# Performance work log

Hardware: AMD Instinct MI355X
Metric: run time of the kernel (lower is better)

The kernel has to match this reference:

```python
import jax, jax.numpy as jnp
import numpy as np

N = 100000      # nodes
E = 1600000     # directed edges
F_IN = 9        # atom features (fixed by GCNConv(9, hidden))
H = 128         # hidden_channels
G = 64          # graphs in batch


def setup_inputs() -> dict:
    key = jax.random.key(0)
    ks = jax.random.split(key, 12)
    x = jax.random.normal(ks[0], (N, F_IN), dtype=jnp.float32)
    edge_index = jax.random.randint(ks[1], (2, E), 0, N, dtype=jnp.int64)
    batch = jnp.sort(jax.random.randint(ks[2], (N,), 0, G, dtype=jnp.int64))
    def lin_init(k, fan_in, fan_out):
        s = 1.0 / np.sqrt(fan_in)
        kw, kb = jax.random.split(k)
        W = jax.random.uniform(kw, (fan_in, fan_out), jnp.float32, -s, s)
        b = jax.random.uniform(kb, (fan_out,), jnp.float32, -s, s)
        return W, b
    W1, b1 = lin_init(ks[3], F_IN, H)
    W2, b2 = lin_init(ks[4], H, H)
    W3, b3 = lin_init(ks[5], H, H)
    lin_w, lin_b = lin_init(ks[6], H, 1)
    return {"x": x, "edge_index": edge_index, "batch": batch,
            "W1": W1, "b1": b1, "W2": W2, "b2": b2, "W3": W3, "b3": b3,
            "lin_w": lin_w, "lin_b": lin_b}


def reference(x, edge_index, batch, W1, b1, W2, b2, W3, b3, lin_w, lin_b):
    n = x.shape[0]
    # PyG GCNConv default: add self-loops, symmetric normalization D^-1/2 (A+I) D^-1/2
    loops = jnp.arange(n, dtype=edge_index.dtype)
    src = jnp.concatenate([edge_index[0], loops])   # [E+N]
    dst = jnp.concatenate([edge_index[1], loops])   # [E+N]
    deg = jax.ops.segment_sum(jnp.ones_like(dst, dtype=x.dtype), dst, num_segments=n)
    dinv = jnp.where(deg > 0, jax.lax.rsqrt(jnp.maximum(deg, 1e-12)), 0.0)
    norm = (dinv[src] * dinv[dst])[:, None]         # [E+N, 1]

    def gcn_conv(h, W, b):
        hw = h @ W                                   # [N, H]
        msg = hw[src] * norm                         # gather + scale  [E+N, H]
        return jax.ops.segment_sum(msg, dst, num_segments=n) + b  # scatter-add

    h = jax.nn.relu(gcn_conv(x, W1, b1))
    h = jax.nn.relu(gcn_conv(h, W2, b2))
    h = gcn_conv(h, W3, b3)

    # global_mean_pool over graph ids
    counts = jax.ops.segment_sum(jnp.ones((n,), x.dtype), batch, num_segments=G)
    pooled = jax.ops.segment_sum(h, batch, num_segments=G) / jnp.maximum(counts, 1.0)[:, None]
    return pooled @ lin_w + lin_b                    # [G, 1]
```

## Files before the change

kernel.cpp:

```cpp
#include <hip/hip_runtime.h>
#include <math.h>


#define CHUNK 2048

using short8 = __attribute__((ext_vector_type(8))) short;
using floatx4 = __attribute__((ext_vector_type(4))) float;

__device__ __forceinline__ int rankof(int i, int nq, int nr) {
  int c = i & 7;
  return c * nq + min(c, nr) + (i >> 3);
}
__device__ __forceinline__ unsigned int f2bf(float f) {
  unsigned int u = __float_as_uint(f);
  return ((u + 0x7fff + ((u >> 16) & 1)) >> 16);
}
__device__ __forceinline__ float bflo(unsigned int u) { return __uint_as_float(u << 16); }
__device__ __forceinline__ float bfhi(unsigned int u) { return __uint_as_float(u & 0xffff0000u); }


__global__ void deg_kernel(const int* __restrict__ dst, int* cnt_rank,
                           int E, int nq, int nr) {
  int e = blockIdx.x * blockDim.x + threadIdx.x;
  if (e < E) atomicAdd(&cnt_rank[rankof(dst[e], nq, nr)], 1);
}

__global__ void dinv_bsum_pad_kernel(const int* __restrict__ cnt_rank,
                                     float* __restrict__ dinv, int* bsum,
                                     const float* __restrict__ x,
                                     unsigned short* __restrict__ xp, int N, int nq, int nr) {
  __shared__ int s[256];
  int t = threadIdx.x;
  int gid = blockIdx.x * 256 + t;
  s[t] = (gid < N) ? cnt_rank[gid] : 0;
  if (gid < N) {
    int c = cnt_rank[rankof(gid, nq, nr)];
    float di = 1.0f / sqrtf((float)c + 1.0f);
    dinv[gid] = di;
    const float* xr = x + (size_t)gid * 9;
    unsigned int w0 = f2bf(xr[0] * di) | (f2bf(xr[1] * di) << 16);
    unsigned int w1 = f2bf(xr[2] * di) | (f2bf(xr[3] * di) << 16);
    unsigned int w2 = f2bf(xr[4] * di) | (f2bf(xr[5] * di) << 16);
    unsigned int w3 = f2bf(xr[6] * di) | (f2bf(xr[7] * di) << 16);
    unsigned int w4 = f2bf(xr[8] * di);
    uint4* xo = (uint4*)(xp + (size_t)gid * 16);
    xo[0] = make_uint4(w0, w1, w2, w3);
    xo[1] = make_uint4(w4, 0u, 0u, 0u);
  }
  __syncthreads();
  for (int off = 128; off > 0; off >>= 1) {
    if (t < off) s[t] += s[t + off];
    __syncthreads();
  }
  if (t == 0) bsum[blockIdx.x] = s[0];
}

__global__ void rowptr_vc0_kernel(const int* __restrict__ indeg, const int* __restrict__ bsum,
                                  int2* __restrict__ rows, int* cursor, int N, int E,
                                  int nq, int nr,
                                  const float* __restrict__ W3, const float* __restrict__ b3,
                                  const float* __restrict__ lin_w, const float* __restrict__ lin_b,
                                  const float* __restrict__ W2, unsigned short* __restrict__ W2p,
                                  unsigned short* __restrict__ g,
                                  float* v, float* c0) {
  __shared__ int ps[256];
  __shared__ int s[256];
  int t = threadIdx.x;
  int pref = 0;
  for (int q = t; q < blockIdx.x; q += 256) pref += bsum[q];
  ps[t] = pref;
  __syncthreads();
  for (int off = 128; off > 0; off >>= 1) {
    if (t < off) ps[t] += ps[t + off];
    __syncthreads();
  }
  int base = ps[0];
  int r = blockIdx.x * 256 + t;
  int val = (r < N) ? indeg[r] : 0;
  s[t] = val;
  __syncthreads();
  for (int off = 1; off < 256; off <<= 1) {
    int x = (t >= off) ? s[t - off] : 0;
    __syncthreads();
    s[t] += x;
    __syncthreads();
  }
  int excl = s[t] - val + base;
  if (r < N) {
    cursor[r] = excl;
    int c = 0;
#pragma unroll
    for (int cc = 1; cc < 8; ++cc) {
      int b = cc * nq + min(cc, nr);
      if (r >= b) c = cc;
    }
    int iinv = ((r - (c * nq + min(c, nr))) << 3) | c;
    rows[iinv] = make_int2(excl, excl + val);
  }
  if (blockIdx.x == 0) {
    if (t < 64) ((unsigned int*)g)[(size_t)N * 64 + t] = 0u;
    if (t < 128) {
      float sv = 0.0f;
      for (int c = 0; c < 128; ++c) sv = fmaf(W3[t * 128 + c], lin_w[c], sv);
      v[t] = sv;
    } else if (t == 128) {
      float sv = 0.0f;
      for (int c = 0; c < 128; ++c) sv = fmaf(b3[c], lin_w[c], sv);
      c0[0] = sv + lin_b[0];
    }
  } else if (blockIdx.x <= 8) {
    int ntile = blockIdx.x - 1;
    int kstep = t >> 6, lane = t & 63;
    int n = ntile * 16 + (lane & 15);
    int k0 = kstep * 32 + ((lane >> 4) & 3) * 8;
    unsigned int pk[4];
#pragma unroll
    for (int jj = 0; jj < 4; ++jj)
      pk[jj] = f2bf(W2[(size_t)(k0 + 2 * jj) * 128 + n])
             | (f2bf(W2[(size_t)(k0 + 2 * jj + 1) * 128 + n]) << 16);
    *(uint4*)(W2p + (size_t)(((ntile * 4 + kstep) * 64 + lane) * 8)) =
        make_uint4(pk[0], pk[1], pk[2], pk[3]);
  }
}

__global__ __launch_bounds__(256) void fill_part_kernel(const int* __restrict__ src,
                                                        const int* __restrict__ dst,
                                                        int* cursor, int* __restrict__ col,
                                                        int E, int nq, int nr) {
  int sub = blockIdx.x & 7;
  int base = (blockIdx.x >> 3) * CHUNK;
#pragma unroll
  for (int j = 0; j < CHUNK / 256; ++j) {
    int e = base + j * 256 + threadIdx.x;
    if (e < E) {
      int d = dst[e];
      if ((d & 7) == sub) {
        int p = atomicAdd(&cursor[rankof(d, nq, nr)], 1);
        col[p] = src[e];
      }
    }
  }
}


__global__ __launch_bounds__(256) void agg9_gemm1_kernel(const unsigned short* __restrict__ xp,
    const float* __restrict__ dinv, const int2* __restrict__ rows,
    const int* __restrict__ col, const float* __restrict__ W1,
    const float* __restrict__ b1, unsigned short* __restrict__ hA, int N) {
  __shared__ float sW[9 * 128];
  __shared__ float sx[128 * 9];
  __shared__ float sdi[128];
  int tid = threadIdx.x;
  for (int q = tid; q < 9 * 128; q += 256) sW[q] = W1[q];
  int nl = tid >> 1;
  int sl = tid & 1;
  int i = blockIdx.x * 128 + nl;
  float A[9], B[9];
#pragma unroll
  for (int f = 0; f < 9; ++f) { A[f] = 0.0f; B[f] = 0.0f; }
  float di = 0.0f;
  if (i < N) {
    di = dinv[i];
    if (sl == 0) {
      const unsigned short* xi = xp + (size_t)i * 16;
      uint4 s0 = *(const uint4*)xi;
      unsigned int s1 = *(const unsigned int*)(xi + 8);
      A[0] = bflo(s0.x); A[1] = bfhi(s0.x); A[2] = bflo(s0.y); A[3] = bfhi(s0.y);
      A[4] = bflo(s0.z); A[5] = bfhi(s0.z); A[6] = bflo(s0.w); A[7] = bfhi(s0.w);
      A[8] = bflo(s1);
    }
    int2 rw = rows[i];
    int re = rw.y;
    int e = rw.x + sl;
    for (; e + 2 < re; e += 4) {
      int c0 = __builtin_nontemporal_load(&col[e]);
      int c1 = __builtin_nontemporal_load(&col[e + 2]);
      const unsigned short* p0 = xp + (size_t)c0 * 16;
      const unsigned short* p1 = xp + (size_t)c1 * 16;
      uint4 q0 = *(const uint4*)p0;
      unsigned int t0 = *(const unsigned int*)(p0 + 8);
      uint4 q1 = *(const uint4*)p1;
      unsigned int t1 = *(const unsigned int*)(p1 + 8);
      A[0] += bflo(q0.x); A[1] += bfhi(q0.x); A[2] += bflo(q0.y); A[3] += bfhi(q0.y);
      A[4] += bflo(q0.z); A[5] += bfhi(q0.z); A[6] += bflo(q0.w); A[7] += bfhi(q0.w);
      A[8] += bflo(t0);
      B[0] += bflo(q1.x); B[1] += bfhi(q1.x); B[2] += bflo(q1.y); B[3] += bfhi(q1.y);
      B[4] += bflo(q1.z); B[5] += bfhi(q1.z); B[6] += bflo(q1.w); B[7] += bfhi(q1.w);
      B[8] += bflo(t1);
    }
    for (; e < re; e += 2) {
      int c0 = __builtin_nontemporal_load(&col[e]);
      const unsigned short* p0 = xp + (size_t)c0 * 16;
      uint4 q0 = *(const uint4*)p0;
      unsigned int t0 = *(const unsigned int*)(p0 + 8);
      A[0] += bflo(q0.x); A[1] += bfhi(q0.x); A[2] += bflo(q0.y); A[3] += bfhi(q0.y);
      A[4] += bflo(q0.z); A[5] += bfhi(q0.z); A[6] += bflo(q0.w); A[7] += bfhi(q0.w);
      A[8] += bflo(t0);
    }
  }
#pragma unroll
  for (int f = 0; f < 9; ++f) {
    float tsum = A[f] + B[f];
    tsum += __shfl_xor(tsum, 1, 64);
    A[f] = tsum;
  }
  if (sl == 0) {
    float* so = sx + nl * 9;
#pragma unroll
    for (int f = 0; f < 9; ++f) so[f] = A[f] * di;
    sdi[nl] = di;
  }
  __syncthreads();
  int c2i = tid & 63, rsub = tid >> 6;
  float wA[9], wB[9];
#pragma unroll
  for (int f = 0; f < 9; ++f) {
    wA[f] = sW[f * 128 + 2 * c2i];
    wB[f] = sW[f * 128 + 2 * c2i + 1];
  }
  float biasA = b1[2 * c2i], biasB = b1[2 * c2i + 1];
  int base = blockIdx.x * 128;
  for (int j = 0; j < 32; ++j) {
    int rl = j * 4 + rsub;
    int row = base + rl;
    if (row >= N) break;
    float sA = biasA, sB = biasB;
#pragma unroll
    for (int f = 0; f < 9; ++f) {
      float xv = sx[rl * 9 + f];
      sA = fmaf(xv, wA[f], sA);
      sB = fmaf(xv, wB[f], sB);
    }
    float d = sdi[rl];
    unsigned int pk = f2bf(fmaxf(sA, 0.0f) * d) | (f2bf(fmaxf(sB, 0.0f) * d) << 16);
    *(unsigned int*)(hA + (size_t)row * 128 + 2 * c2i) = pk;
  }
}


__global__ __launch_bounds__(256) void aggH_kernel(const unsigned short* __restrict__ h,
    const int2* __restrict__ rows, const int* __restrict__ col,
    unsigned short* __restrict__ g, int N) {
  int wave = threadIdx.x >> 6;
  int lane = threadIdx.x & 63;
  int half = lane >> 5;
  int l32  = lane & 31;
  int i = blockIdx.x * 4 + wave;
  if (i >= N) return;
  uint2 sp = *((const uint2*)(h + (size_t)i * 128) + l32);
  float m = half ? 0.0f : 1.0f;
  float4 a0 = make_float4(bflo(sp.x) * m, bfhi(sp.x) * m, bflo(sp.y) * m, bfhi(sp.y) * m);
  float4 a1 = make_float4(0.f, 0.f, 0.f, 0.f);
  float4 a2 = make_float4(0.f, 0.f, 0.f, 0.f);
  float4 a3 = make_float4(0.f, 0.f, 0.f, 0.f);
  int2 rw = rows[i];
  int rs = rw.x, re = rw.y;
  int e = rs;
  for (; e + 8 <= re; e += 8) {
    int c0 = __builtin_nontemporal_load(&col[e + half]);
    int c1 = __builtin_nontemporal_load(&col[e + 2 + half]);
    int c2 = __builtin_nontemporal_load(&col[e + 4 + half]);
    int c3 = __builtin_nontemporal_load(&col[e + 6 + half]);
    uint2 p0 = *((const uint2*)(h + (size_t)c0 * 128) + l32);
    uint2 p1 = *((const uint2*)(h + (size_t)c1 * 128) + l32);
    uint2 p2 = *((const uint2*)(h + (size_t)c2 * 128) + l32);
    uint2 p3 = *((const uint2*)(h + (size_t)c3 * 128) + l32);
    a0.x += bflo(p0.x); a0.y += bfhi(p0.x); a0.z += bflo(p0.y); a0.w += bfhi(p0.y);
    a1.x += bflo(p1.x); a1.y += bfhi(p1.x); a1.z += bflo(p1.y); a1.w += bfhi(p1.y);
    a2.x += bflo(p2.x); a2.y += bfhi(p2.x); a2.z += bflo(p2.y); a2.w += bfhi(p2.y);
    a3.x += bflo(p3.x); a3.y += bfhi(p3.x); a3.z += bflo(p3.y); a3.w += bfhi(p3.y);
  }
  if (e + 4 <= re) {
    int c0 = __builtin_nontemporal_load(&col[e + half]);
    int c1 = __builtin_nontemporal_load(&col[e + 2 + half]);
    uint2 p0 = *((const uint2*)(h + (size_t)c0 * 128) + l32);
    uint2 p1 = *((const uint2*)(h + (size_t)c1 * 128) + l32);
    a0.x += bflo(p0.x); a0.y += bfhi(p0.x); a0.z += bflo(p0.y); a0.w += bfhi(p0.y);
    a1.x += bflo(p1.x); a1.y += bfhi(p1.x); a1.z += bflo(p1.y); a1.w += bfhi(p1.y);
    e += 4;
  }
  if (e + 2 <= re) {
    int c0 = __builtin_nontemporal_load(&col[e + half]);
    uint2 p0 = *((const uint2*)(h + (size_t)c0 * 128) + l32);
    a2.x += bflo(p0.x); a2.y += bfhi(p0.x); a2.z += bflo(p0.y); a2.w += bfhi(p0.y);
    e += 2;
  }
  if (e < re) {
    int c0 = __builtin_nontemporal_load(&col[e]);
    uint2 p0 = *((const uint2*)(h + (size_t)c0 * 128) + l32);
    a3.x = fmaf(bflo(p0.x), 0.5f, a3.x); a3.y = fmaf(bfhi(p0.x), 0.5f, a3.y);
    a3.z = fmaf(bflo(p0.y), 0.5f, a3.z); a3.w = fmaf(bfhi(p0.y), 0.5f, a3.w);
  }
  float4 a = make_float4((a0.x + a1.x) + (a2.x + a3.x), (a0.y + a1.y) + (a2.y + a3.y),
                         (a0.z + a1.z) + (a2.z + a3.z), (a0.w + a1.w) + (a2.w + a3.w));
  a.x += __shfl_down(a.x, 32, 64);
  a.y += __shfl_down(a.y, 32, 64);
  a.z += __shfl_down(a.z, 32, 64);
  a.w += __shfl_down(a.w, 32, 64);
  if (half == 0) {
    uint2 o;
    o.x = f2bf(a.x) | (f2bf(a.y) << 16);
    o.y = f2bf(a.z) | (f2bf(a.w) << 16);
    *((uint2*)(g + (size_t)i * 128) + l32) = o;
  }
}


__global__ __launch_bounds__(256) void gemmz_kernel(const unsigned short* __restrict__ g,
    const unsigned short* __restrict__ W2p, const float* __restrict__ dinv,
    const float* __restrict__ b2, const float* __restrict__ v,
    float* __restrict__ zd, int N) {
  int wave = threadIdx.x >> 6, lane = threadIdx.x & 63;
  int rb16 = blockIdx.x * 64 + wave * 16;
  int m = lane & 15, quad = lane >> 4;
  int rowA = rb16 + m;
  const unsigned short* gp = g + (size_t)((rowA < N) ? rowA : N) * 128 + quad * 8;
  floatx4 acc[8];
#pragma unroll
  for (int t = 0; t < 8; ++t) acc[t] = (floatx4){0.f, 0.f, 0.f, 0.f};
#pragma unroll
  for (int ks = 0; ks < 4; ++ks) {
    short8 afrag = *(const short8*)(gp + ks * 32);
#pragma unroll
    for (int t = 0; t < 8; ++t) {
      short8 bfrag = *(const short8*)(W2p + (size_t)(((t * 4 + ks) * 64 + lane) * 8));
      acc[t] = __builtin_amdgcn_mfma_f32_16x16x32_bf16(afrag, bfrag, acc[t], 0, 0, 0);
    }
  }
  float b2c[8], vc[8];
#pragma unroll
  for (int t = 0; t < 8; ++t) {
    int ncol = t * 16 + m;
    b2c[t] = b2[ncol];
    vc[t] = v[ncol];
  }
#pragma unroll
  for (int reg = 0; reg < 4; ++reg) {
    int grow = rb16 + quad * 4 + reg;
    float dr = (grow < N) ? dinv[grow] : 0.0f;
    float p = 0.0f;
#pragma unroll
    for (int t = 0; t < 8; ++t)
      p += fmaxf(fmaf(dr, acc[t][reg], b2c[t]), 0.0f) * vc[t];
#pragma unroll
    for (int mk = 1; mk <= 8; mk <<= 1) p += __shfl_xor(p, mk, 64);
    if (m == 0 && grow < N) zd[grow] = dr * p;
  }
}


__global__ void agg1_pool_kernel(const float* __restrict__ zd, const float* __restrict__ dinv,
    const int2* __restrict__ rows, const int* __restrict__ col,
    const int* __restrict__ batch, float* gsum, float* gcnt, int N) {
  __shared__ float lsum[64];
  __shared__ float lcnt[64];
  int t = threadIdx.x;
  if (t < 64) { lsum[t] = 0.0f; lcnt[t] = 0.0f; }
  __syncthreads();
  int nl = t >> 1, sl = t & 1;
  int i = blockIdx.x * 128 + nl;
  float acc = 0.0f;
  if (i < N) {
    int2 rw = rows[i];
    int re = rw.y;
    if (sl == 0) acc = zd[i];
    int e = rw.x + sl;
    for (; e + 2 < re; e += 4) {
      float z0 = zd[col[e]], z1 = zd[col[e + 2]];
      acc += z0 + z1;
    }
    for (; e < re; e += 2) acc += zd[col[e]];
  }
  acc += __shfl_xor(acc, 1, 64);
  if (i < N && sl == 0) {
    acc *= dinv[i];
    int gidx = batch[i];
    atomicAdd(&lsum[gidx], acc);
    atomicAdd(&lcnt[gidx], 1.0f);
  }
  __syncthreads();
  if (t < 64) {
    if (lsum[t] != 0.0f) atomicAdd(&gsum[t], lsum[t]);
    if (lcnt[t] != 0.0f) atomicAdd(&gcnt[t], lcnt[t]);
  }
}

__global__ void final_kernel(const float* __restrict__ gsum, const float* __restrict__ gcnt,
                             const float* __restrict__ c0, float* out, int G) {
  int g = threadIdx.x;
  if (g < G) out[g] = gsum[g] / fmaxf(gcnt[g], 1.0f) + c0[0];
}


extern "C" void kernel_launch(void* const* d_in, const int* in_sizes, int n_in,
                              void* d_out, int out_size, void* d_ws, size_t ws_size,
                              hipStream_t stream) {
  const float* x      = (const float*)d_in[0];
  const int*   eidx   = (const int*)d_in[1];
  const int*   batch  = (const int*)d_in[2];
  const float* W1     = (const float*)d_in[3];
  const float* b1     = (const float*)d_in[4];
  const float* W2     = (const float*)d_in[5];
  const float* b2     = (const float*)d_in[6];
  const float* W3     = (const float*)d_in[7];
  const float* b3     = (const float*)d_in[8];
  const float* lin_w  = (const float*)d_in[9];
  const float* lin_b  = (const float*)d_in[10];
  float* out = (float*)d_out;

  int N = in_sizes[0] / 9;
  int E = in_sizes[1] / 2;
  int G = out_size;
  const int* src = eidx;
  const int* dst = eidx + E;
  int nq = N >> 3, nr = N & 7;

  char* w = (char*)d_ws;
  size_t off = 0;
  auto alloc = [&](size_t bytes) -> void* {
    void* p = w + off;
    off += bytes;
    off = (off + 255) & ~(size_t)255;
    return p;
  };

  int nb = (N + 255) / 256;
  int nb2 = (N + 127) / 128;
  int nchunk = (E + CHUNK - 1) / CHUNK;
  int*   cursor = (int*)  alloc((size_t)N * 4);
  float* gsum   = (float*)alloc(64 * 4);
  float* gcnt   = (float*)alloc(64 * 4);
  size_t zspan = off;
  float* dinv   = (float*)alloc((size_t)N * 4);
  int2*  rows   = (int2*) alloc((size_t)N * 8);
  int*   bsum   = (int*)  alloc((size_t)nb * 4);
  int*   colsrc = (int*)  alloc((size_t)E * 4);
  unsigned short* hA  = (unsigned short*)alloc((size_t)N * 128 * 2);
  unsigned short* g   = (unsigned short*)alloc((size_t)(N + 1) * 128 * 2);
  unsigned short* W2p = (unsigned short*)alloc(8 * 4 * 64 * 8 * 2);
  float* zd     = (float*)alloc((size_t)N * 4);
  float* v      = (float*)alloc(128 * 4);
  float* c0     = (float*)alloc(4);
  unsigned short* xp = g;

  hipMemsetAsync(d_ws, 0, zspan, stream);
  deg_kernel<<<(E + 255) / 256, 256, 0, stream>>>(dst, cursor, E, nq, nr);
  dinv_bsum_pad_kernel<<<nb, 256, 0, stream>>>(cursor, dinv, bsum, x, xp, N, nq, nr);
  rowptr_vc0_kernel<<<nb, 256, 0, stream>>>(cursor, bsum, rows, cursor, N, E, nq, nr,
                                            W3, b3, lin_w, lin_b, W2, W2p, g, v, c0);
  fill_part_kernel<<<nchunk * 8, 256, 0, stream>>>(src, dst, cursor, colsrc, E, nq, nr);
  agg9_gemm1_kernel<<<nb2, 256, 0, stream>>>(xp, dinv, rows, colsrc, W1, b1, hA, N);
  aggH_kernel<<<(N + 3) / 4, 256, 0, stream>>>(hA, rows, colsrc, g, N);
  gemmz_kernel<<<(N + 63) / 64, 256, 0, stream>>>(g, W2p, dinv, b2, v, zd, N);
  agg1_pool_kernel<<<nb2, 256, 0, stream>>>(zd, dinv, rows, colsrc, batch, gsum, gcnt, N);
  final_kernel<<<1, 64, 0, stream>>>(gsum, gcnt, c0, out, G);
}
```

Before: 363.4 us.

## Pre-bucket edges by destination class before CSR fill

```diff
diff --git a/kernel.cpp b/kernel.cpp
--- a/kernel.cpp
+++ b/kernel.cpp
@@ -19,10 +19,36 @@
 __device__ __forceinline__ float bfhi(unsigned int u) { return __uint_as_float(u & 0xffff0000u); }
 
 
-__global__ void deg_kernel(const int* __restrict__ dst, int* cnt_rank,
-                           int E, int nq, int nr) {
-  int e = blockIdx.x * blockDim.x + threadIdx.x;
-  if (e < E) atomicAdd(&cnt_rank[rankof(dst[e], nq, nr)], 1);
+__global__ __launch_bounds__(256) void bucket_kernel(const int* __restrict__ src,
+    const int* __restrict__ dst, int* cnt_rank, int* clsCount,
+    uint2* __restrict__ ebuf, int segCap, int E, int nq, int nr) {
+  __shared__ int cnt[8];
+  __shared__ int base[8];
+  int t = threadIdx.x;
+  if (t < 8) cnt[t] = 0;
+  __syncthreads();
+  int e0 = blockIdx.x * CHUNK;
+  int d[8], s[8], off[8];
+#pragma unroll
+  for (int j = 0; j < 8; ++j) {
+    int e = e0 + j * 256 + t;
+    if (e < E) {
+      d[j] = dst[e]; s[j] = src[e];
+      off[j] = atomicAdd(&cnt[d[j] & 7], 1);
+    } else d[j] = -1;
+  }
+  __syncthreads();
+  if (t < 8) base[t] = atomicAdd(&clsCount[t], cnt[t]);
+  __syncthreads();
+#pragma unroll
+  for (int j = 0; j < 8; ++j) {
+    if (d[j] >= 0) {
+      int c = d[j] & 7;
+      ebuf[(size_t)c * segCap + base[c] + off[j]] =
+          make_uint2((unsigned)d[j], (unsigned)s[j]);
+      atomicAdd(&cnt_rank[rankof(d[j], nq, nr)], 1);
+    }
+  }
 }
 
 __global__ void dinv_bsum_pad_kernel(const int* __restrict__ cnt_rank,
@@ -123,21 +149,21 @@
   }
 }
 
-__global__ __launch_bounds__(256) void fill_part_kernel(const int* __restrict__ src,
-                                                        const int* __restrict__ dst,
-                                                        int* cursor, int* __restrict__ col,
-                                                        int E, int nq, int nr) {
+__global__ __launch_bounds__(256) void fill_seg_kernel(const uint2* __restrict__ ebuf,
+                                                       const int* __restrict__ clsCount,
+                                                       int segCap, int* cursor,
+                                                       int* __restrict__ col, int nq, int nr) {
   int sub = blockIdx.x & 7;
-  int base = (blockIdx.x >> 3) * CHUNK;
+  int start = (blockIdx.x >> 3) * CHUNK;
+  int count = clsCount[sub];
+  const uint2* seg = ebuf + (size_t)sub * segCap;
 #pragma unroll
   for (int j = 0; j < CHUNK / 256; ++j) {
-    int e = base + j * 256 + threadIdx.x;
-    if (e < E) {
-      int d = dst[e];
-      if ((d & 7) == sub) {
-        int p = atomicAdd(&cursor[rankof(d, nq, nr)], 1);
-        col[p] = src[e];
-      }
+    int e = start + j * 256 + threadIdx.x;
+    if (e < count) {
+      uint2 p = seg[e];
+      int pos = atomicAdd(&cursor[rankof((int)p.x, nq, nr)], 1);
+      col[pos] = (int)p.y;
     }
   }
 }
@@ -427,14 +453,18 @@
   int nb = (N + 255) / 256;
   int nb2 = (N + 127) / 128;
   int nchunk = (E + CHUNK - 1) / CHUNK;
-  int*   cursor = (int*)  alloc((size_t)N * 4);
-  float* gsum   = (float*)alloc(64 * 4);
-  float* gcnt   = (float*)alloc(64 * 4);
+  int segCap = E / 8 + 65536;
+  int nseg = (segCap + CHUNK - 1) / CHUNK;
+  int*   cursor   = (int*)  alloc((size_t)N * 4);
+  float* gsum     = (float*)alloc(64 * 4);
+  float* gcnt     = (float*)alloc(64 * 4);
+  int*   clsCount = (int*)  alloc(8 * 4);
   size_t zspan = off;
   float* dinv   = (float*)alloc((size_t)N * 4);
   int2*  rows   = (int2*) alloc((size_t)N * 8);
   int*   bsum   = (int*)  alloc((size_t)nb * 4);
   int*   colsrc = (int*)  alloc((size_t)E * 4);
+  uint2* ebuf   = (uint2*)alloc((size_t)segCap * 8 * 8);
   unsigned short* hA  = (unsigned short*)alloc((size_t)N * 128 * 2);
   unsigned short* g   = (unsigned short*)alloc((size_t)(N + 1) * 128 * 2);
   unsigned short* W2p = (unsigned short*)alloc(8 * 4 * 64 * 8 * 2);
@@ -444,11 +474,11 @@
   unsigned short* xp = g;
 
   hipMemsetAsync(d_ws, 0, zspan, stream);
-  deg_kernel<<<(E + 255) / 256, 256, 0, stream>>>(dst, cursor, E, nq, nr);
+  bucket_kernel<<<nchunk, 256, 0, stream>>>(src, dst, cursor, clsCount, ebuf, segCap, E, nq, nr);
   dinv_bsum_pad_kernel<<<nb, 256, 0, stream>>>(cursor, dinv, bsum, x, xp, N, nq, nr);
   rowptr_vc0_kernel<<<nb, 256, 0, stream>>>(cursor, bsum, rows, cursor, N, E, nq, nr,
                                             W3, b3, lin_w, lin_b, W2, W2p, g, v, c0);
-  fill_part_kernel<<<nchunk * 8, 256, 0, stream>>>(src, dst, cursor, colsrc, E, nq, nr);
+  fill_seg_kernel<<<nseg * 8, 256, 0, stream>>>(ebuf, clsCount, segCap, cursor, colsrc, nq, nr);
   agg9_gemm1_kernel<<<nb2, 256, 0, stream>>>(xp, dinv, rows, colsrc, W1, b1, hA, N);
   aggH_kernel<<<(N + 3) / 4, 256, 0, stream>>>(hA, rows, colsrc, g, N);
   gemmz_kernel<<<(N + 63) / 64, 256, 0, stream>>>(g, W2p, dinv, b2, v, zd, N);
```

New measurement: 376.6 us. +3.6%, slower.
